# Kernel tuning notes

Hardware: AMD Instinct MI355X
Metric: run time of the kernel (lower is better)

Reference implementation:

```python
import jax, jax.numpy as jnp
import numpy as np

DECAY = 0.99
EPS = 1e-5  # Laplace smoothing eps in cluster-size balancing


def _quantize(z_flat, embedding, cluster_size, emb_avg, n_codes):
    # z_flat: [N, D]; embedding: [K, D]
    d = (jnp.sum(z_flat * z_flat, axis=1, keepdims=True)
         + jnp.sum(embedding * embedding, axis=1)
         - 2.0 * (z_flat @ embedding.T))                      # [N, K]
    idx = jnp.argmin(d, axis=1)                               # [N]
    # EMA update (training path). segment_sum == one-hot matmul scatter-add.
    counts = jax.ops.segment_sum(jnp.ones(z_flat.shape[0], z_flat.dtype), idx,
                                 num_segments=n_codes)        # [K]
    new_cs = cluster_size * DECAY + (1.0 - DECAY) * counts
    dw = jax.ops.segment_sum(z_flat, idx, num_segments=n_codes)  # [K, D]
    new_avg = emb_avg * DECAY + (1.0 - DECAY) * dw
    n = new_cs.sum()
    bal = (new_cs + EPS) / (n + n_codes * EPS) * n
    # torch assigns via .data (no autograd) -> stop_gradient for faithfulness
    new_emb = jax.lax.stop_gradient(new_avg / bal[:, None])
    z_q = jnp.take(new_emb, idx, axis=0)  # == one_hot(idx) @ new_emb
    return idx, z_q


def _l2norm(x):
    # F.normalize(x, dim=-1) with eps=1e-12
    return x / jnp.maximum(jnp.linalg.norm(x, axis=-1, keepdims=True), 1e-12)


def reference(z, structure_embedding, style_embedding,
              structure_cluster_size, style_cluster_size,
              structure_embedding_avg, style_embedding_avg):
    b, c, h, w, d = z.shape
    zp = jnp.transpose(z, (0, 2, 3, 4, 1))      # b h w d c
    z_flat = zp.reshape(-1, c)                  # [N, D]
    s_idx, s_q = _quantize(z_flat, structure_embedding, structure_cluster_size,
                           structure_embedding_avg, structure_embedding.shape[0])
    y_idx, y_q = _quantize(z_flat, style_embedding, style_cluster_size,
                           style_embedding_avg, style_embedding.shape[0])

    def back(q):  # [N, C] -> b c h w d
        return jnp.transpose(q.reshape(b, h, w, d, c), (0, 4, 1, 2, 3))

    s_enc = back(s_q)
    y_enc = back(y_q)
    # NOTE: faithful to source — normalize over LAST axis of (b,c,h,w,d),
    # i.e. the spatial depth axis, exactly as F.normalize(dim=-1) does there.
    dis = jnp.mean(jnp.sum(_l2norm(s_enc) * _l2norm(y_enc), axis=-1) ** 2)
    z_q = (s_enc + y_enc) * 0.5
    return z_q, dis, s_idx, y_idx


def setup_inputs() -> dict:
    key = jax.random.key(0)
    k1, k2, k3 = jax.random.split(key, 3)
    B, C, H, W, D = 16, 256, 16, 16, 16
    Ks, Ky = 1024, 512
    return {
        "z": jax.random.normal(k1, (B, C, H, W, D), dtype=jnp.float32),
        "structure_embedding": jax.random.normal(k2, (Ks, C), dtype=jnp.float32),
        "style_embedding": jax.random.normal(k3, (Ky, C), dtype=jnp.float32),
        "structure_cluster_size": jnp.zeros((Ks,), jnp.float32),
        "style_cluster_size": jnp.zeros((Ky,), jnp.float32),
        "structure_embedding_avg": jnp.zeros((Ks, C), jnp.float32),
        "style_embedding_avg": jnp.zeros((Ky, C), jnp.float32),
    }
```

## Files before the change

kernel.cpp:

```cpp
#include <hip/hip_runtime.h>
#include <float.h>

#define NROWS 65536
#define CDIM  256
#define KS    1024
#define KY    512
#define KTOT  1536
#define SPB   4096

#define WB_CNT_S       0
#define WB_CNT_Y       4096
#define WB_RESCUE_CNT  6144
#define WB_DISACC      6152
#define WB_DW_S        6400
#define WB_DW_Y        1054976
#define WB_ZERO_BYTES  1579264
#define WB_EIMG        1579264
#define WB_EN2         2365696
#define WB_IDXS_I      2371840
#define WB_IDXY_I      2633984
#define WB_RLIST_S     2896128
#define WB_RLIST_Y     3158272
#define WB_BASE_S      3420416
#define WB_BASE_Y      3424512
#define WB_CUR_S       3426560
#define WB_CUR_Y       3430656
#define WB_SCALE_S     3432704
#define WB_SCALE_Y     3436800
#define WB_PERM_S      3438848
#define WB_PERM_Y      3700992
#define WB_KSORT_S     3963136
#define WB_KSORT_Y     4225280
#define WB_EMB_S       4487424
#define WB_EMB_Y       5536000

#define OFF_OUT_ZQ   0
#define OFF_OUT_DIS  16777216
#define OFF_OUT_SIDX 16777217
#define OFF_OUT_YIDX 16842753

typedef __attribute__((ext_vector_type(8)))  _Float16 f16x8;
typedef __attribute__((ext_vector_type(16))) float    f32x16;

__device__ __forceinline__ unsigned int umn(unsigned int a, unsigned int b) { return a < b ? a : b; }
__device__ __forceinline__ unsigned int umx(unsigned int a, unsigned int b) { return a > b ? a : b; }

__global__ void prep_e(const float* __restrict__ Es, const float* __restrict__ Ey,
                       unsigned short* __restrict__ eimg, float* __restrict__ en2) {
    int k = blockIdx.x;
    int lane = threadIdx.x;
    const float* E = (k < KS) ? (Es + (size_t)k * CDIM) : (Ey + (size_t)(k - KS) * CDIM);
    float4 v = *(const float4*)(E + lane * 4);
    float nrm = v.x * v.x + v.y * v.y + v.z * v.z + v.w * v.w;
#pragma unroll
    for (int off = 32; off > 0; off >>= 1) nrm += __shfl_down(nrm, off);
    if (lane == 0) en2[k] = nrm;

    unsigned short q0 = __builtin_bit_cast(unsigned short, (_Float16)v.x);
    unsigned short q1 = __builtin_bit_cast(unsigned short, (_Float16)v.y);
    unsigned short q2 = __builtin_bit_cast(unsigned short, (_Float16)v.z);
    unsigned short q3 = __builtin_bit_cast(unsigned short, (_Float16)v.w);
    uint2 hp = make_uint2((unsigned)q0 | ((unsigned)q1 << 16),
                          (unsigned)q2 | ((unsigned)q3 << 16));

    int t = k >> 5, kin = k & 31;
    int cc = lane >> 2, g = (lane >> 1) & 1, j0 = (lane & 1) * 4;
    size_t base = (size_t)t * 8192 + (size_t)(cc * 512) + (size_t)((kin + 32 * g) * 8 + j0);
    *(uint2*)(eimg + base) = hp;
}

__global__ void prep_z(const float* __restrict__ z, float* __restrict__ zf) {
    __shared__ float Zs[32][257];
    int blk = blockIdx.x;
    int n0 = blk * 32, b = n0 >> 12, s0 = n0 & 4095;
    int t = threadIdx.x;
    const float* zb = z + (size_t)b * CDIM * SPB + s0;
#pragma unroll
    for (int i = 0; i < 32; ++i) {
        int l = i * 256 + t;
        int c = l >> 5, s = l & 31;
        Zs[s][c] = zb[(size_t)c * SPB + s];
    }
    __syncthreads();
#pragma unroll
    for (int j = 0; j < 8; ++j) {
        int gid = j * 256 + t;
        int nl = gid >> 6, fg = gid & 63;
        float4 v = *(const float4*)(&Zs[nl][fg * 4]);
        *(float4*)(&zf[(size_t)(n0 + nl) * 256 + fg * 4]) = v;
    }
}

__device__ __forceinline__ void stage_chunk(const unsigned short* __restrict__ eimg,
                                            int t, unsigned short* lsbase,
                                            int wave, int lane) {
    const char* gs = (const char*)eimg + (size_t)t * 16384 + wave * 8192 + lane * 16;
    char* ls = (char*)lsbase + wave * 8192;
#pragma unroll
    for (int i = 0; i < 8; ++i)
        __builtin_amdgcn_global_load_lds(
            (const __attribute__((address_space(1))) void*)(gs + i * 1024),
            (__attribute__((address_space(3))) void*)(ls + i * 1024), 16, 0, 0);
}

__launch_bounds__(128, 2)
__global__ void assign_kernel(const float* __restrict__ z, const unsigned short* __restrict__ eimg,
                              const float* __restrict__ en2,
                              float* __restrict__ sidx_f, float* __restrict__ yidx_f,
                              int* __restrict__ sidx_i, int* __restrict__ yidx_i,
                              int* __restrict__ cnt_s, int* __restrict__ cnt_y,
                              int* __restrict__ rescue_cnt,
                              int* __restrict__ rlist_s, int* __restrict__ rlist_y) {
    __shared__ unsigned short sh[2][8192];
    const int tid = threadIdx.x, wave = tid >> 6, lane = tid & 63;
    const int row32 = lane & 31;
    const int n0 = blockIdx.x * 64;
    const int b = n0 >> 12;
    const int myrow_s = (n0 & 4095) + wave * 32 + row32;
    const float* zb = z + (size_t)b * CDIM * SPB;
    const int g8 = (lane >> 5) * 8;

    stage_chunk(eimg, 0, &sh[0][0], wave, lane);

    f16x8 Ah[16];
#pragma unroll
    for (int cc = 0; cc < 16; ++cc) {
        f16x8 a;
#pragma unroll
        for (int j = 0; j < 8; ++j)
            a[j] = (_Float16)zb[(size_t)(cc * 16 + g8 + j) * SPB + myrow_s];
        Ah[cc] = a;
    }

    unsigned int m1[16], m2[16];
#pragma unroll
    for (int i = 0; i < 16; ++i) { m1[i] = 0xFFFFFFFFu; m2[i] = 0xFFFFFFFFu; }

    for (int t = 0; t < 48; ++t) {
        unsigned short* cur = &sh[t & 1][0];
        if (t + 1 < 48) {
            stage_chunk(eimg, t + 1, &sh[(t + 1) & 1][0], wave, lane);
            asm volatile("s_waitcnt vmcnt(8)" ::: "memory");
        } else {
            asm volatile("s_waitcnt vmcnt(0)" ::: "memory");
        }
        __builtin_amdgcn_s_barrier();
        asm volatile("" ::: "memory");

        const int kglob = t * 32 + row32;
        const float en0 = en2[kglob] + 512.0f;
        f32x16 acc = {};
        const char* shb = (const char*)cur + lane * 16;
#pragma unroll
        for (int cc = 0; cc < 16; ++cc) {
            f16x8 bh = *(const f16x8*)(shb + cc * 1024);
            acc = __builtin_amdgcn_mfma_f32_32x32x16_f16(Ah[cc], bh, acc, 0, 0, 0);
        }
        const unsigned int tag = (unsigned int)kglob;
#pragma unroll
        for (int i = 0; i < 16; ++i) {
            float d = fmaf(-2.f, acc[i], en0);
            unsigned int du = (__float_as_uint(d) & 0xFFFFF800u) | tag;
            m2[i] = umn(m2[i], umx(m1[i], du));
            m1[i] = umn(m1[i], du);
        }
        asm volatile("s_waitcnt lgkmcnt(0)" ::: "memory");
        __builtin_amdgcn_s_barrier();
        asm volatile("" ::: "memory");

        if (t == 31 || t == 47) {
            const int book = (t == 47);
            float* fo = book ? yidx_f : sidx_f;
            int*   io = book ? yidx_i : sidx_i;
            int*   cb = book ? cnt_y : cnt_s;
            int*   rl = book ? rlist_y : rlist_s;
#pragma unroll
            for (int i = 0; i < 16; ++i) {
                unsigned int v1 = m1[i], v2 = m2[i];
#pragma unroll
                for (int m = 16; m >= 1; m >>= 1) {
                    unsigned int o1 = (unsigned int)__shfl_xor((int)v1, m);
                    unsigned int o2 = (unsigned int)__shfl_xor((int)v2, m);
                    v2 = umn(umn(v2, o2), umx(v1, o1));
                    v1 = umn(v1, o1);
                }
                if (row32 == 0) {
                    int kw  = (int)(v1 & 0x7FFu) - (book ? KS : 0);
                    int k2w = (int)(v2 & 0x7FFu) - (book ? KS : 0);
                    int r = (i & 3) + 8 * (i >> 2) + 4 * (lane >> 5);
                    int n = n0 + wave * 32 + r;
                    fo[n] = (float)kw;
                    io[n] = kw;
                    atomicAdd(&cb[kw], 1);
                    if ((v1 >> 11) + 4 > (v2 >> 11)) {
                        int p = atomicAdd(&rescue_cnt[book], 1);
                        if (p < 65536) rl[p] = n | (k2w << 16);
                    }
                }
            }
            if (t == 31) {
#pragma unroll
                for (int i = 0; i < 16; ++i) { m1[i] = 0xFFFFFFFFu; m2[i] = 0xFFFFFFFFu; }
            }
        }
    }
}

__global__ void rescue2_kernel(const float* __restrict__ zf, const float* __restrict__ E,
                               const float* __restrict__ en2k,
                               const int* __restrict__ rcnt, const int* __restrict__ rlist,
                               float* __restrict__ idx_f, int* __restrict__ idx_i,
                               int* __restrict__ cnt) {
    int ce = *rcnt; if (ce > 65536) ce = 65536;
    const int lane = threadIdx.x & 63;
    const int nw = (gridDim.x * blockDim.x) >> 6;
    for (int e = (int)((blockIdx.x * blockDim.x + threadIdx.x) >> 6); e < ce; e += nw) {
        unsigned int ent = (unsigned int)rlist[e];
        int n  = (int)(ent & 0xFFFFu);
        int k2 = (int)(ent >> 16);
        int k1 = idx_i[n];
        float4 zv = *(const float4*)(zf + (size_t)n * 256 + lane * 4);
        float4 a  = *(const float4*)(E + (size_t)k1 * 256 + lane * 4);
        float4 c  = *(const float4*)(E + (size_t)k2 * 256 + lane * 4);
        float d1 = zv.x * a.x + zv.y * a.y + zv.z * a.z + zv.w * a.w;
        float d2 = zv.x * c.x + zv.y * c.y + zv.z * c.z + zv.w * c.w;
#pragma unroll
        for (int off = 32; off > 0; off >>= 1) {
            d1 += __shfl_down(d1, off);
            d2 += __shfl_down(d2, off);
        }
        if (lane == 0) {
            float dist1 = en2k[k1] - 2.f * d1;
            float dist2 = en2k[k2] - 2.f * d2;
            int nk = (dist2 < dist1 || (dist2 == dist1 && k2 < k1)) ? k2 : k1;
            if (nk != k1) {
                atomicSub(&cnt[k1], 1);
                atomicAdd(&cnt[nk], 1);
                idx_i[n] = nk;
                idx_f[n] = (float)nk;
            }
        }
    }
}

__global__ void scanbal_kernel(const float* __restrict__ cs_in, const float* __restrict__ cy_in,
                               const int* __restrict__ cnt_s, const int* __restrict__ cnt_y,
                               int* __restrict__ base_s, int* __restrict__ base_y,
                               int* __restrict__ cur_s, int* __restrict__ cur_y,
                               float* __restrict__ scale_s, float* __restrict__ scale_y) {
    __shared__ int   sc[1024];
    __shared__ float sf[1024];
    int K = blockIdx.x ? KY : KS;
    const float* csi = blockIdx.x ? cy_in : cs_in;
    const int*   cnt = blockIdx.x ? cnt_y : cnt_s;
    int* base = blockIdx.x ? base_y : base_s;
    int* cur  = blockIdx.x ? cur_y  : cur_s;
    float* scale = blockIdx.x ? scale_y : scale_s;
    int t = threadIdx.x;
    int c = (t < K) ? cnt[t] : 0;
    float ncs = (t < K) ? (csi[t] * 0.99f + 0.01f * (float)c) : 0.f;
    sc[t] = c;
    __syncthreads();
    for (int off = 1; off < 1024; off <<= 1) {
        int v = sc[t] + ((t >= off) ? sc[t - off] : 0);
        __syncthreads();
        sc[t] = v;
        __syncthreads();
    }
    int incl = sc[t];
    sf[t] = ncs;
    __syncthreads();
    for (int s2 = 512; s2 > 0; s2 >>= 1) {
        if (t < s2) sf[t] += sf[t + s2];
        __syncthreads();
    }
    float nsum = sf[0];
    if (t < K) {
        base[t] = incl - c;
        cur[t]  = incl - c;
        float bal = (ncs + 1e-5f) / (nsum + (float)K * 1e-5f) * nsum;
        scale[t] = 1.0f / bal;
    }
}

__global__ void scatter_kernel(const int* __restrict__ si, const int* __restrict__ yi,
                               int* __restrict__ cur_s, int* __restrict__ cur_y,
                               int* __restrict__ perm_s, int* __restrict__ perm_y,
                               int* __restrict__ ksort_s, int* __restrict__ ksort_y) {
    int i = blockIdx.x * 256 + threadIdx.x;
    if (i < NROWS) {
        int k = si[i]; int p = atomicAdd(&cur_s[k], 1);
        perm_s[p] = i; ksort_s[p] = k;
    } else {
        int n = i - NROWS; int k = yi[n]; int p = atomicAdd(&cur_y[k], 1);
        perm_y[p] = n; ksort_y[p] = k;
    }
}

__global__ void dw_kernel(const float* __restrict__ zf,
                          const int* __restrict__ perm_s, const int* __restrict__ ksort_s,
                          const int* __restrict__ perm_y, const int* __restrict__ ksort_y,
                          float* __restrict__ dw_s, float* __restrict__ dw_y) {
    __shared__ int keys[33];
    __shared__ int rows[32];
    const int t = threadIdx.x;
    int blk = blockIdx.x;
    const int* perm; const int* ks; float* dw; int p0;
    if (blk < NROWS / 32) { perm = perm_s; ks = ksort_s; dw = dw_s; p0 = blk * 32; }
    else                  { perm = perm_y; ks = ksort_y; dw = dw_y; p0 = (blk - NROWS / 32) * 32; }
    if (t < 32) { keys[t] = ks[p0 + t]; rows[t] = perm[p0 + t]; }
    if (t == 32) keys[32] = -1;
    __syncthreads();
    float acc = 0.f;
#pragma unroll 8
    for (int j = 0; j < 32; ++j) {
        acc += zf[(size_t)rows[j] * 256 + t];
        if (keys[j + 1] != keys[j]) {
            atomicAdd(&dw[(size_t)keys[j] * 256 + t], acc);
            acc = 0.f;
        }
    }
}

__global__ void embnew_kernel(const float* __restrict__ avg_s, const float* __restrict__ avg_y,
                              const float* __restrict__ dw_s, const float* __restrict__ dw_y,
                              const float* __restrict__ scale_s, const float* __restrict__ scale_y,
                              float* __restrict__ emb_s, float* __restrict__ emb_y) {
    int id = blockIdx.x, t = threadIdx.x;
    if (id < KS) { int i = id * 256 + t; emb_s[i] = (avg_s[i] * 0.99f + 0.01f * dw_s[i]) * scale_s[id]; }
    else { int kk = id - KS; int i = kk * 256 + t; emb_y[i] = (avg_y[i] * 0.99f + 0.01f * dw_y[i]) * scale_y[kk]; }
}

__global__ void gather_kernel(const float* __restrict__ Se, const float* __restrict__ Ye,
                              const int* __restrict__ sidx, const int* __restrict__ yidx,
                              float* __restrict__ zq, float* __restrict__ disacc) {
    __shared__ float qb[256 * 17];
    __shared__ int   si[16], yi[16];
    __shared__ float red[256];
    const int g  = blockIdx.x;
    const int b  = g >> 8;
    const int hw = g & 255;
    const int t  = threadIdx.x;
    if (t < 16) {
        int n = b * SPB + hw * 16 + t;
        si[t] = sidx[n];
        yi[t] = yidx[n];
    }
    __syncthreads();
    float ns = 0.f, ny = 0.f, dot = 0.f;
#pragma unroll
    for (int d = 0; d < 16; ++d) {
        float s = Se[(size_t)si[d] * CDIM + t];
        float y = Ye[(size_t)yi[d] * CDIM + t];
        ns  = fmaf(s, s, ns);
        ny  = fmaf(y, y, ny);
        dot = fmaf(s, y, dot);
        qb[t * 17 + d] = 0.5f * (s + y);
    }
    float den = fmaxf(sqrtf(ns), 1e-12f) * fmaxf(sqrtf(ny), 1e-12f);
    float val = dot / den;
    red[t] = val * val;
    __syncthreads();
    for (int s = 128; s > 0; s >>= 1) {
        if (t < s) red[t] += red[t + s];
        __syncthreads();
    }
    if (t == 0) atomicAdd(disacc, red[0]);
    float* zg = zq + (size_t)b * CDIM * SPB + hw * 16;
#pragma unroll
    for (int j = 0; j < 16; ++j) {
        int e = j * 256 + t;
        int c = e >> 4, d = e & 15;
        zg[(size_t)c * SPB + d] = qb[c * 17 + d];
    }
}

__global__ void fin_kernel(const float* __restrict__ disacc, float* __restrict__ out_dis) {
    *out_dis = *disacc * (1.0f / 1048576.0f);
}

extern "C" void kernel_launch(void* const* d_in, const int* in_sizes, int n_in,
                              void* d_out, int out_size, void* d_ws, size_t ws_size,
                              hipStream_t stream) {
    const float* z     = (const float*)d_in[0];
    const float* Es    = (const float*)d_in[1];
    const float* Ey    = (const float*)d_in[2];
    const float* s_cs  = (const float*)d_in[3];
    const float* y_cs  = (const float*)d_in[4];
    const float* s_avg = (const float*)d_in[5];
    const float* y_avg = (const float*)d_in[6];
    float* out = (float*)d_out;
    char*  w   = (char*)d_ws;

    unsigned short* eimg = (unsigned short*)(w + WB_EIMG);
    float* en2    = (float*)(w + WB_EN2);
    int* idxs_i   = (int*)(w + WB_IDXS_I);
    int* idxy_i   = (int*)(w + WB_IDXY_I);
    int* cnt_s    = (int*)(w + WB_CNT_S);
    int* cnt_y    = (int*)(w + WB_CNT_Y);
    int* r_cnt    = (int*)(w + WB_RESCUE_CNT);
    int* rlist_s  = (int*)(w + WB_RLIST_S);
    int* rlist_y  = (int*)(w + WB_RLIST_Y);
    int* base_s   = (int*)(w + WB_BASE_S);
    int* base_y   = (int*)(w + WB_BASE_Y);
    int* cur_s    = (int*)(w + WB_CUR_S);
    int* cur_y    = (int*)(w + WB_CUR_Y);
    float* scale_s = (float*)(w + WB_SCALE_S);
    float* scale_y = (float*)(w + WB_SCALE_Y);
    int* perm_s   = (int*)(w + WB_PERM_S);
    int* perm_y   = (int*)(w + WB_PERM_Y);
    int* ksort_s  = (int*)(w + WB_KSORT_S);
    int* ksort_y  = (int*)(w + WB_KSORT_Y);
    float* dw_s   = (float*)(w + WB_DW_S);
    float* dw_y   = (float*)(w + WB_DW_Y);
    float* emb_s  = (float*)(w + WB_EMB_S);
    float* emb_y  = (float*)(w + WB_EMB_Y);

    float* zf     = out + OFF_OUT_ZQ;
    float* sidx_f = out + OFF_OUT_SIDX;
    float* yidx_f = out + OFF_OUT_YIDX;

    hipMemsetAsync(w, 0, WB_ZERO_BYTES, stream);

    prep_e<<<KTOT, 64, 0, stream>>>(Es, Ey, eimg, en2);
    prep_z<<<NROWS / 32, 256, 0, stream>>>(z, zf);

    assign_kernel<<<NROWS / 64, 128, 0, stream>>>(z, eimg, en2, sidx_f, yidx_f,
                                                  idxs_i, idxy_i, cnt_s, cnt_y,
                                                  r_cnt, rlist_s, rlist_y);

    rescue2_kernel<<<512, 256, 0, stream>>>(zf, Es, en2, r_cnt, rlist_s,
                                            sidx_f, idxs_i, cnt_s);
    rescue2_kernel<<<512, 256, 0, stream>>>(zf, Ey, en2 + KS, r_cnt + 1, rlist_y,
                                            yidx_f, idxy_i, cnt_y);

    scanbal_kernel<<<2, 1024, 0, stream>>>(s_cs, y_cs, cnt_s, cnt_y, base_s, base_y,
                                           cur_s, cur_y, scale_s, scale_y);
    scatter_kernel<<<2 * NROWS / 256, 256, 0, stream>>>(idxs_i, idxy_i, cur_s, cur_y,
                                                        perm_s, perm_y, ksort_s, ksort_y);
    dw_kernel<<<2 * NROWS / 32, 256, 0, stream>>>(zf, perm_s, ksort_s, perm_y, ksort_y, dw_s, dw_y);
    embnew_kernel<<<KTOT, 256, 0, stream>>>(s_avg, y_avg, dw_s, dw_y, scale_s, scale_y, emb_s, emb_y);
    gather_kernel<<<4096, 256, 0, stream>>>(emb_s, emb_y, idxs_i, idxy_i,
                                            out + OFF_OUT_ZQ, (float*)(w + WB_DISACC));
    fin_kernel<<<1, 1, 0, stream>>>((float*)(w + WB_DISACC), out + OFF_OUT_DIS);
}
```

Before: 339.0 us.

## Split assign kernel codebook across wave pairs with 16x16 MFMA tiles

Rewrites the distance/argmin kernel to use 256-thread blocks where two wave pairs each scan half of the 1536 combined codes, using 16x16x32 MFMA with each wave holding two 16-row A tiles. The codebook image layout is changed to match 16-code chunks, and A operands are now loaded from the already-transposed zf buffer with vector loads instead of strided reads from z. Partial top-2 results for structure codes are merged through shared memory across pairs. The two rescue launches are also fused into one. The intent is more parallelism per block and less load latency, at the cost of cross-wave merging and higher register and LDS use per block.

```diff
diff --git a/kernel.cpp b/kernel.cpp
--- a/kernel.cpp
+++ b/kernel.cpp
@@ -40,7 +40,7 @@
 #define OFF_OUT_YIDX 16842753
 
 typedef __attribute__((ext_vector_type(8)))  _Float16 f16x8;
-typedef __attribute__((ext_vector_type(16))) float    f32x16;
+typedef __attribute__((ext_vector_type(4)))  float    f32x4;
 
 __device__ __forceinline__ unsigned int umn(unsigned int a, unsigned int b) { return a < b ? a : b; }
 __device__ __forceinline__ unsigned int umx(unsigned int a, unsigned int b) { return a > b ? a : b; }
@@ -63,10 +63,11 @@
     uint2 hp = make_uint2((unsigned)q0 | ((unsigned)q1 << 16),
                           (unsigned)q2 | ((unsigned)q3 << 16));
 
-    int t = k >> 5, kin = k & 31;
-    int cc = lane >> 2, g = (lane >> 1) & 1, j0 = (lane & 1) * 4;
-    size_t base = (size_t)t * 8192 + (size_t)(cc * 512) + (size_t)((kin + 32 * g) * 8 + j0);
-    *(uint2*)(eimg + base) = hp;
+    int c0 = lane * 4;
+    int kc = c0 >> 5, g = (c0 >> 3) & 3, j0 = c0 & 7;
+    size_t byteoff = (size_t)(k >> 4) * 8192 + (size_t)kc * 1024
+                   + (size_t)(g * 16 + (k & 15)) * 16 + (size_t)j0 * 2;
+    *(uint2*)((char*)eimg + byteoff) = hp;
 }
 
 __global__ void prep_z(const float* __restrict__ z, float* __restrict__ zf) {
@@ -91,133 +92,199 @@
     }
 }
 
-__device__ __forceinline__ void stage_chunk(const unsigned short* __restrict__ eimg,
-                                            int t, unsigned short* lsbase,
-                                            int wave, int lane) {
-    const char* gs = (const char*)eimg + (size_t)t * 16384 + wave * 8192 + lane * 16;
-    char* ls = (char*)lsbase + wave * 8192;
-#pragma unroll
-    for (int i = 0; i < 8; ++i)
+__device__ __forceinline__ void stage4(const unsigned short* __restrict__ eimg,
+                                       int chunk, char* lsbase, int wrow, int lane) {
+    const char* gs = (const char*)eimg + (size_t)chunk * 8192 + wrow * 4096 + lane * 16;
+    char* ls = lsbase + wrow * 4096;
+#pragma unroll
+    for (int i = 0; i < 4; ++i)
         __builtin_amdgcn_global_load_lds(
             (const __attribute__((address_space(1))) void*)(gs + i * 1024),
             (__attribute__((address_space(3))) void*)(ls + i * 1024), 16, 0, 0);
 }
 
-__launch_bounds__(128, 2)
-__global__ void assign_kernel(const float* __restrict__ z, const unsigned short* __restrict__ eimg,
+__launch_bounds__(256, 3)
+__global__ void assign_kernel(const float* __restrict__ zf, const unsigned short* __restrict__ eimg,
                               const float* __restrict__ en2,
                               float* __restrict__ sidx_f, float* __restrict__ yidx_f,
                               int* __restrict__ sidx_i, int* __restrict__ yidx_i,
                               int* __restrict__ cnt_s, int* __restrict__ cnt_y,
                               int* __restrict__ rescue_cnt,
                               int* __restrict__ rlist_s, int* __restrict__ rlist_y) {
-    __shared__ unsigned short sh[2][8192];
+    __shared__ char shraw[32768];
+    __shared__ unsigned int mv1[64], mv2[64];
     const int tid = threadIdx.x, wave = tid >> 6, lane = tid & 63;
-    const int row32 = lane & 31;
+    const int pair = wave >> 1, wrow = wave & 1;
     const int n0 = blockIdx.x * 64;
-    const int b = n0 >> 12;
-    const int myrow_s = (n0 & 4095) + wave * 32 + row32;
-    const float* zb = z + (size_t)b * CDIM * SPB;
-    const int g8 = (lane >> 5) * 8;
-
-    stage_chunk(eimg, 0, &sh[0][0], wave, lane);
-
-    f16x8 Ah[16];
-#pragma unroll
-    for (int cc = 0; cc < 16; ++cc) {
-        f16x8 a;
-#pragma unroll
-        for (int j = 0; j < 8; ++j)
-            a[j] = (_Float16)zb[(size_t)(cc * 16 + g8 + j) * SPB + myrow_s];
-        Ah[cc] = a;
-    }
-
-    unsigned int m1[16], m2[16];
-#pragma unroll
-    for (int i = 0; i < 16; ++i) { m1[i] = 0xFFFFFFFFu; m2[i] = 0xFFFFFFFFu; }
-
-    for (int t = 0; t < 48; ++t) {
-        unsigned short* cur = &sh[t & 1][0];
-        if (t + 1 < 48) {
-            stage_chunk(eimg, t + 1, &sh[(t + 1) & 1][0], wave, lane);
-            asm volatile("s_waitcnt vmcnt(8)" ::: "memory");
+    char* shp = shraw + pair * 16384;
+
+    stage4(eimg, pair * 48, shp, wrow, lane);
+
+    f16x8 A[2][8];
+#pragma unroll
+    for (int rg = 0; rg < 2; ++rg) {
+        const float* zr = zf + (size_t)(n0 + wrow * 32 + rg * 16 + (lane & 15)) * 256
+                        + (lane >> 4) * 8;
+#pragma unroll
+        for (int kc = 0; kc < 8; ++kc) {
+            float4 f0 = *(const float4*)(zr + kc * 32);
+            float4 f1 = *(const float4*)(zr + kc * 32 + 4);
+            f16x8 a;
+            a[0] = (_Float16)f0.x; a[1] = (_Float16)f0.y;
+            a[2] = (_Float16)f0.z; a[3] = (_Float16)f0.w;
+            a[4] = (_Float16)f1.x; a[5] = (_Float16)f1.y;
+            a[6] = (_Float16)f1.z; a[7] = (_Float16)f1.w;
+            A[rg][kc] = a;
+        }
+    }
+
+    unsigned int m1a[2][4], m2a[2][4];
+#pragma unroll
+    for (int rg = 0; rg < 2; ++rg)
+#pragma unroll
+        for (int q = 0; q < 4; ++q) { m1a[rg][q] = 0xFFFFFFFFu; m2a[rg][q] = 0xFFFFFFFFu; }
+
+    for (int i = 0; i < 48; ++i) {
+        const int chunk = pair * 48 + i;
+        if (i + 1 < 48) {
+            stage4(eimg, chunk + 1, shp + ((i + 1) & 1) * 8192, wrow, lane);
+            asm volatile("s_waitcnt vmcnt(4)" ::: "memory");
         } else {
             asm volatile("s_waitcnt vmcnt(0)" ::: "memory");
         }
         __builtin_amdgcn_s_barrier();
         asm volatile("" ::: "memory");
 
-        const int kglob = t * 32 + row32;
-        const float en0 = en2[kglob] + 512.0f;
-        f32x16 acc = {};
-        const char* shb = (const char*)cur + lane * 16;
-#pragma unroll
-        for (int cc = 0; cc < 16; ++cc) {
-            f16x8 bh = *(const f16x8*)(shb + cc * 1024);
-            acc = __builtin_amdgcn_mfma_f32_32x32x16_f16(Ah[cc], bh, acc, 0, 0, 0);
-        }
-        const unsigned int tag = (unsigned int)kglob;
-#pragma unroll
-        for (int i = 0; i < 16; ++i) {
-            float d = fmaf(-2.f, acc[i], en0);
-            unsigned int du = (__float_as_uint(d) & 0xFFFFF800u) | tag;
-            m2[i] = umn(m2[i], umx(m1[i], du));
-            m1[i] = umn(m1[i], du);
+        const char* bb = shp + (i & 1) * 8192 + lane * 16;
+        f32x4 acc0 = {}, acc1 = {};
+#pragma unroll
+        for (int kc = 0; kc < 8; ++kc) {
+            f16x8 B = *(const f16x8*)(bb + kc * 1024);
+            acc0 = __builtin_amdgcn_mfma_f32_16x16x32_f16(A[0][kc], B, acc0, 0, 0, 0);
+            acc1 = __builtin_amdgcn_mfma_f32_16x16x32_f16(A[1][kc], B, acc1, 0, 0, 0);
+        }
+        const int kcode = chunk * 16 + (lane & 15);
+        const float en0 = en2[kcode] + 512.0f;
+        const unsigned int tag = (unsigned int)kcode;
+#pragma unroll
+        for (int q = 0; q < 4; ++q) {
+            float d0 = fmaf(-2.f, acc0[q], en0);
+            unsigned int du0 = (__float_as_uint(d0) & 0xFFFFF800u) | tag;
+            m2a[0][q] = umn(m2a[0][q], umx(m1a[0][q], du0));
+            m1a[0][q] = umn(m1a[0][q], du0);
+            float d1 = fmaf(-2.f, acc1[q], en0);
+            unsigned int du1 = (__float_as_uint(d1) & 0xFFFFF800u) | tag;
+            m2a[1][q] = umn(m2a[1][q], umx(m1a[1][q], du1));
+            m1a[1][q] = umn(m1a[1][q], du1);
         }
         asm volatile("s_waitcnt lgkmcnt(0)" ::: "memory");
         __builtin_amdgcn_s_barrier();
         asm volatile("" ::: "memory");
 
-        if (t == 31 || t == 47) {
-            const int book = (t == 47);
-            float* fo = book ? yidx_f : sidx_f;
-            int*   io = book ? yidx_i : sidx_i;
-            int*   cb = book ? cnt_y : cnt_s;
-            int*   rl = book ? rlist_y : rlist_s;
-#pragma unroll
-            for (int i = 0; i < 16; ++i) {
-                unsigned int v1 = m1[i], v2 = m2[i];
-#pragma unroll
-                for (int m = 16; m >= 1; m >>= 1) {
+        if (pair == 1 && i == 15) {
+#pragma unroll
+            for (int rg = 0; rg < 2; ++rg)
+#pragma unroll
+                for (int q = 0; q < 4; ++q) {
+                    unsigned int v1 = m1a[rg][q], v2 = m2a[rg][q];
+#pragma unroll
+                    for (int m = 8; m >= 1; m >>= 1) {
+                        unsigned int o1 = (unsigned int)__shfl_xor((int)v1, m);
+                        unsigned int o2 = (unsigned int)__shfl_xor((int)v2, m);
+                        v2 = umn(umn(v2, o2), umx(v1, o1));
+                        v1 = umn(v1, o1);
+                    }
+                    if ((lane & 15) == 0) {
+                        int r64 = wrow * 32 + rg * 16 + (lane >> 4) * 4 + q;
+                        mv1[r64] = v1; mv2[r64] = v2;
+                    }
+                    m1a[rg][q] = 0xFFFFFFFFu; m2a[rg][q] = 0xFFFFFFFFu;
+                }
+        }
+    }
+
+    if (pair == 0) {
+#pragma unroll
+        for (int rg = 0; rg < 2; ++rg)
+#pragma unroll
+            for (int q = 0; q < 4; ++q) {
+                unsigned int v1 = m1a[rg][q], v2 = m2a[rg][q];
+#pragma unroll
+                for (int m = 8; m >= 1; m >>= 1) {
                     unsigned int o1 = (unsigned int)__shfl_xor((int)v1, m);
                     unsigned int o2 = (unsigned int)__shfl_xor((int)v2, m);
                     v2 = umn(umn(v2, o2), umx(v1, o1));
                     v1 = umn(v1, o1);
                 }
-                if (row32 == 0) {
-                    int kw  = (int)(v1 & 0x7FFu) - (book ? KS : 0);
-                    int k2w = (int)(v2 & 0x7FFu) - (book ? KS : 0);
-                    int r = (i & 3) + 8 * (i >> 2) + 4 * (lane >> 5);
-                    int n = n0 + wave * 32 + r;
-                    fo[n] = (float)kw;
-                    io[n] = kw;
-                    atomicAdd(&cb[kw], 1);
-                    if ((v1 >> 11) + 4 > (v2 >> 11)) {
-                        int p = atomicAdd(&rescue_cnt[book], 1);
-                        if (p < 65536) rl[p] = n | (k2w << 16);
+                if ((lane & 15) == 0) {
+                    int r64 = wrow * 32 + rg * 16 + (lane >> 4) * 4 + q;
+                    unsigned int p1 = mv1[r64], p2 = mv2[r64];
+                    unsigned int nv2 = umn(umn(v2, p2), umx(v1, p1));
+                    unsigned int nv1 = umn(v1, p1);
+                    int kw = (int)(nv1 & 0x7FFu);
+                    int n = n0 + r64;
+                    sidx_f[n] = (float)kw;
+                    sidx_i[n] = kw;
+                    atomicAdd(&cnt_s[kw], 1);
+                    if ((nv1 >> 11) + 4 > (nv2 >> 11)) {
+                        int k2w = (int)(nv2 & 0x7FFu);
+                        int p = atomicAdd(&rescue_cnt[0], 1);
+                        if (p < 65536) rlist_s[p] = n | (k2w << 16);
                     }
                 }
             }
-            if (t == 31) {
-#pragma unroll
-                for (int i = 0; i < 16; ++i) { m1[i] = 0xFFFFFFFFu; m2[i] = 0xFFFFFFFFu; }
+    } else {
+#pragma unroll
+        for (int rg = 0; rg < 2; ++rg)
+#pragma unroll
+            for (int q = 0; q < 4; ++q) {
+                unsigned int v1 = m1a[rg][q], v2 = m2a[rg][q];
+#pragma unroll
+                for (int m = 8; m >= 1; m >>= 1) {
+                    unsigned int o1 = (unsigned int)__shfl_xor((int)v1, m);
+                    unsigned int o2 = (unsigned int)__shfl_xor((int)v2, m);
+                    v2 = umn(umn(v2, o2), umx(v1, o1));
+                    v1 = umn(v1, o1);
+                }
+                if ((lane & 15) == 0) {
+                    int r64 = wrow * 32 + rg * 16 + (lane >> 4) * 4 + q;
+                    int kw = (int)(v1 & 0x7FFu) - KS;
+                    int n = n0 + r64;
+                    yidx_f[n] = (float)kw;
+                    yidx_i[n] = kw;
+                    atomicAdd(&cnt_y[kw], 1);
+                    if ((v1 >> 11) + 4 > (v2 >> 11)) {
+                        int k2w = (int)(v2 & 0x7FFu) - KS;
+                        int p = atomicAdd(&rescue_cnt[1], 1);
+                        if (p < 65536) rlist_y[p] = n | (k2w << 16);
+                    }
+                }
             }
-        }
-    }
-}
-
-__global__ void rescue2_kernel(const float* __restrict__ zf, const float* __restrict__ E,
-                               const float* __restrict__ en2k,
-                               const int* __restrict__ rcnt, const int* __restrict__ rlist,
-                               float* __restrict__ idx_f, int* __restrict__ idx_i,
-                               int* __restrict__ cnt) {
-    int ce = *rcnt; if (ce > 65536) ce = 65536;
+    }
+}
+
+__global__ void rescue2_kernel(const float* __restrict__ zf,
+                               const float* __restrict__ Es, const float* __restrict__ Ey,
+                               const float* __restrict__ en2, const int* __restrict__ rcnt,
+                               const int* __restrict__ rlist_s, const int* __restrict__ rlist_y,
+                               float* __restrict__ sidx_f, float* __restrict__ yidx_f,
+                               int* __restrict__ sidx_i, int* __restrict__ yidx_i,
+                               int* __restrict__ cnt_s, int* __restrict__ cnt_y) {
+    int cs = rcnt[0]; if (cs > 65536) cs = 65536;
+    int cy = rcnt[1]; if (cy > 65536) cy = 65536;
+    int total = cs + cy;
     const int lane = threadIdx.x & 63;
     const int nw = (gridDim.x * blockDim.x) >> 6;
-    for (int e = (int)((blockIdx.x * blockDim.x + threadIdx.x) >> 6); e < ce; e += nw) {
-        unsigned int ent = (unsigned int)rlist[e];
+    for (int e = (int)((blockIdx.x * blockDim.x + threadIdx.x) >> 6); e < total; e += nw) {
+        int book = (e >= cs);
+        unsigned int ent = (unsigned int)(book ? rlist_y[e - cs] : rlist_s[e]);
         int n  = (int)(ent & 0xFFFFu);
         int k2 = (int)(ent >> 16);
+        int* idx_i = book ? yidx_i : sidx_i;
+        float* idx_f = book ? yidx_f : sidx_f;
+        int* cnt = book ? cnt_y : cnt_s;
+        const float* E = book ? Ey : Es;
+        const float* en2k = book ? (en2 + KS) : en2;
         int k1 = idx_i[n];
         float4 zv = *(const float4*)(zf + (size_t)n * 256 + lane * 4);
         float4 a  = *(const float4*)(E + (size_t)k1 * 256 + lane * 4);
@@ -425,14 +492,12 @@
     prep_e<<<KTOT, 64, 0, stream>>>(Es, Ey, eimg, en2);
     prep_z<<<NROWS / 32, 256, 0, stream>>>(z, zf);
 
-    assign_kernel<<<NROWS / 64, 128, 0, stream>>>(z, eimg, en2, sidx_f, yidx_f,
+    assign_kernel<<<NROWS / 64, 256, 0, stream>>>(zf, eimg, en2, sidx_f, yidx_f,
                                                   idxs_i, idxy_i, cnt_s, cnt_y,
                                                   r_cnt, rlist_s, rlist_y);
 
-    rescue2_kernel<<<512, 256, 0, stream>>>(zf, Es, en2, r_cnt, rlist_s,
-                                            sidx_f, idxs_i, cnt_s);
-    rescue2_kernel<<<512, 256, 0, stream>>>(zf, Ey, en2 + KS, r_cnt + 1, rlist_y,
-                                            yidx_f, idxy_i, cnt_y);
+    rescue2_kernel<<<512, 256, 0, stream>>>(zf, Es, Ey, en2, r_cnt, rlist_s, rlist_y,
+                                            sidx_f, yidx_f, idxs_i, idxy_i, cnt_s, cnt_y);
 
     scanbal_kernel<<<2, 1024, 0, stream>>>(s_cs, y_cs, cnt_s, cnt_y, base_s, base_y,
                                            cur_s, cur_y, scale_s, scale_y);
```

Result: faster. 322.2 us (-5.0%).
